# Performance work log

Measured on AMD Instinct MI355X. Metric: run time of the kernel, lower is better.

## Reference

```python
import jax, jax.numpy as jnp
import numpy as np

H, I, SI, E = 2048, 1408, 5632, 60
B, S = 1, 512


def setup_inputs() -> dict:
    key = jax.random.key(0)
    ks = jax.random.split(key, 9)
    sc = 0.02  # weight init scale for numerical stability
    return {
        "hidden_states": jax.random.normal(ks[0], (B, S, H), dtype=jnp.float32),
        "router_w": jax.random.normal(ks[1], (E, H), dtype=jnp.float32) * sc,
        "gate_w": jax.random.normal(ks[2], (E, I, H), dtype=jnp.float32) * sc,
        "up_w": jax.random.normal(ks[3], (E, I, H), dtype=jnp.float32) * sc,
        "down_w": jax.random.normal(ks[4], (E, H, I), dtype=jnp.float32) * sc,
        "sh_gate_w": jax.random.normal(ks[5], (SI, H), dtype=jnp.float32) * sc,
        "sh_up_w": jax.random.normal(ks[6], (SI, H), dtype=jnp.float32) * sc,
        "sh_down_w": jax.random.normal(ks[7], (H, SI), dtype=jnp.float32) * sc,
        "expert_gate_w": jax.random.normal(ks[8], (1, H), dtype=jnp.float32) * sc,
        "top_k": 4,
    }


NORM_TOPK_PROB = False  # Qwen1.5-MoE config


def reference(hidden_states, router_w, gate_w, up_w, down_w,
              sh_gate_w, sh_up_w, sh_down_w, expert_gate_w, top_k):
    b, s, h = hidden_states.shape
    x = hidden_states.reshape(-1, h)                      # [T, H]

    # --- router: softmax over all experts, then top-k sparse weights ---
    logits = x @ router_w.T                               # [T, E]
    probs = jax.nn.softmax(logits.astype(jnp.float32), axis=-1)
    vals, idx = jax.lax.top_k(probs, top_k)               # [T, k]
    if NORM_TOPK_PROB:
        vals = vals / jnp.sum(vals, axis=-1, keepdims=True)
    # scatter top-k weights back to dense [T, E] (zeros elsewhere)
    onehot = jax.nn.one_hot(idx, E, dtype=probs.dtype)    # [T, k, E]
    w = jnp.einsum('tke,tk->te', onehot, vals).astype(x.dtype)  # [T, E]

    # --- grouped GLU experts (dense-masked faithful reference) ---
    g = jnp.einsum('td,eid->tei', x, gate_w)              # [T, E, I]
    a = jax.nn.silu(g) * jnp.einsum('td,eid->tei', x, up_w)
    moe = jnp.einsum('tei,ehi,te->th', a, down_w, w)      # [T, H]

    # --- shared expert with sigmoid gate ---
    shared = (jax.nn.silu(x @ sh_gate_w.T) * (x @ sh_up_w.T)) @ sh_down_w.T
    shared = jax.nn.sigmoid(x @ expert_gate_w.T) * shared # [T,1]*[T,H]

    return (moe + shared).reshape(b, s, h)
```

## Files before the change

### kernel.cpp

```cpp
#include <hip/hip_runtime.h>
#include <hip/hip_bf16.h>
#include <stdint.h>

#define TOKENS 512
#define HDIM   2048
#define IDIM   1408
#define SIDIM  5632
#define NEXP   60
#define TOPK   4
#define NSLOTS (TOKENS*TOPK)
#define ROWPAD 64

#define VMWAIT(N) asm volatile("s_waitcnt vmcnt(" #N ")" ::: "memory")
#define SBAR()    asm volatile("s_barrier" ::: "memory")

typedef __attribute__((ext_vector_type(8))) short bf16x8;
typedef __attribute__((ext_vector_type(4))) float f32x4;

__device__ __forceinline__ short f2bf(float f){
  uint32_t u = __float_as_uint(f);
  u = (u + 0x7fffu + ((u >> 16) & 1u)) >> 16;
  return (short)(u & 0xffffu);
}

__device__ __forceinline__ bf16x8 pack8(float4 a, float4 b){
  bf16x8 r;
  r[0]=f2bf(a.x); r[1]=f2bf(a.y); r[2]=f2bf(a.z); r[3]=f2bf(a.w);
  r[4]=f2bf(b.x); r[5]=f2bf(b.y); r[6]=f2bf(b.z); r[7]=f2bf(b.w);
  return r;
}

__device__ __forceinline__ bf16x8 as_bf16x8(float4 v){
  union { float4 f; bf16x8 b; } u; u.f = v; return u.b;
}

__device__ __forceinline__ f32x4 zero4(){
  f32x4 z; z[0]=0.f; z[1]=0.f; z[2]=0.f; z[3]=0.f; return z;
}

__device__ __forceinline__ f32x4 mfma16(bf16x8 a, bf16x8 b, f32x4 c){
  return __builtin_amdgcn_mfma_f32_16x16x32_bf16(a, b, c, 0, 0, 0);
}

__device__ __forceinline__ void stage_w32(float4* tile, const float* __restrict__ W,
                                          int K, int k0, int tid){
  int l = tid & 63, wv = tid >> 6;
  #pragma unroll
  for (int j=0;j<2;j++){
    int u0 = j*256 + wv*64;
    int u  = u0 + l;
    int row = u >> 3;
    int lu  = ((u & 7) - (row & 7)) & 7;
    const float* src = W + (size_t)row*K + k0 + lu*4;
    __builtin_amdgcn_global_load_lds(
        (const __attribute__((address_space(1))) void*)src,
        (__attribute__((address_space(3))) void*)(tile + u0), 16, 0, 0);
  }
}

__device__ __forceinline__ bf16x8 read_wfrag32(const float4* tile, int r, int kq){
  int rot = r & 7;
  const float4* row = tile + (size_t)r*8;
  float4 f0 = row[(2*kq     + rot) & 7];
  float4 f1 = row[(2*kq + 1 + rot) & 7];
  return pack8(f0, f1);
}

__device__ __forceinline__ void stage_a32(float4* tile, const short* __restrict__ Arows,
                                          int K, int k0, int tid){
  int l = tid & 63, wv = tid >> 6;
  int u0 = wv*64;
  int u  = u0 + l;
  int row = u >> 2;
  int lu  = ((u & 3) - (row & 3)) & 3;
  const short* src = Arows + (size_t)row*K + k0 + lu*8;
  __builtin_amdgcn_global_load_lds(
      (const __attribute__((address_space(1))) void*)src,
      (__attribute__((address_space(3))) void*)(tile + u0), 16, 0, 0);
}

__device__ __forceinline__ void read_afrag32(const float4* tile, int c16, int kq,
                                             bf16x8* av){
  #pragma unroll
  for (int mf=0; mf<4; mf++){
    int row = c16 + 16*mf;
    av[mf] = as_bf16x8(tile[(size_t)row*4 + ((kq + row) & 3)]);
  }
}

__global__ __launch_bounds__(64) void router_kernel(
    const float* __restrict__ x, const float* __restrict__ rw,
    const float* __restrict__ egw, int* __restrict__ topk_idx,
    float* __restrict__ topk_w, float* __restrict__ gates,
    int* __restrict__ counts)
{
  int t = blockIdx.x;
  int lane = threadIdx.x;
  const float* xr = x + (size_t)t*HDIM;
  float xv[HDIM/64];
  #pragma unroll
  for (int i=0;i<HDIM/64;i++) xv[i] = xr[lane + 64*i];

  float mylogit = -1e30f;
  for (int e=0;e<NEXP;e++){
    const float* w = rw + (size_t)e*HDIM;
    float acc = 0.f;
    #pragma unroll
    for (int i=0;i<HDIM/64;i++) acc += xv[i]*w[lane+64*i];
    #pragma unroll
    for (int s=32;s>0;s>>=1) acc += __shfl_xor(acc, s);
    if (lane == e) mylogit = acc;
  }
  {
    float acc = 0.f;
    #pragma unroll
    for (int i=0;i<HDIM/64;i++) acc += xv[i]*egw[lane+64*i];
    #pragma unroll
    for (int s=32;s>0;s>>=1) acc += __shfl_xor(acc, s);
    if (lane == 0) gates[t] = 1.f/(1.f + __expf(-acc));
  }
  float m = mylogit;
  #pragma unroll
  for (int s=32;s>0;s>>=1) m = fmaxf(m, __shfl_xor(m, s));
  float p = (lane < NEXP) ? __expf(mylogit - m) : 0.f;
  float sum = p;
  #pragma unroll
  for (int s=32;s>0;s>>=1) sum += __shfl_xor(sum, s);
  float prob = p / sum;
  for (int k=0;k<TOPK;k++){
    float v = prob; int idx = lane;
    #pragma unroll
    for (int s=32;s>0;s>>=1){
      float ov = __shfl_xor(v, s); int oi = __shfl_xor(idx, s);
      if (ov > v || (ov == v && oi < idx)){ v = ov; idx = oi; }
    }
    if (lane == 0){
      topk_idx[t*TOPK+k] = idx;
      topk_w[t*TOPK+k]  = v;
      atomicAdd(&counts[idx], 1);
    }
    if (lane == idx) prob = -1e30f;
  }
}

__global__ void prefix_kernel(const int* __restrict__ counts, int* __restrict__ offsets)
{
  if (threadIdx.x == 0){
    int acc = 0;
    for (int e=0;e<NEXP;e++){ offsets[e] = acc; acc += counts[e]; }
    offsets[NEXP] = acc;
  }
}

__global__ __launch_bounds__(256) void scatter_kernel(
    const float* __restrict__ x, const int* __restrict__ topk_idx,
    const int* __restrict__ offsets, int* __restrict__ fill,
    int* __restrict__ slot_of, __hip_bfloat16* __restrict__ xg,
    __hip_bfloat16* __restrict__ xb)
{
  int t = blockIdx.x, tid = threadIdx.x;
  __shared__ int sl[TOPK];
  if (tid == 0){
    for (int k=0;k<TOPK;k++){
      int e = topk_idx[t*TOPK+k];
      int pos = atomicAdd(&fill[e], 1);
      int s = offsets[e] + pos;
      slot_of[t*TOPK+k] = s;
      sl[k] = s;
    }
  }
  __syncthreads();
  const float4* xr = (const float4*)(x + (size_t)t*HDIM);
  float4 v0 = xr[tid*2], v1 = xr[tid*2+1];
  bf16x8 b = pack8(v0, v1);
  *(bf16x8*)((short*)xb + (size_t)t*HDIM + tid*8) = b;
  #pragma unroll
  for (int k=0;k<TOPK;k++)
    *(bf16x8*)((short*)xg + (size_t)sl[k]*HDIM + tid*8) = b;
}

__global__ __launch_bounds__(256, 4) void gateup_all(
    const float* __restrict__ gW_e, const float* __restrict__ uW_e,
    const __hip_bfloat16* __restrict__ A_e, __hip_bfloat16* __restrict__ out_e,
    const float* __restrict__ gW_s, const float* __restrict__ uW_s,
    const __hip_bfloat16* __restrict__ A_s, __hip_bfloat16* __restrict__ out_s,
    const int* __restrict__ offsets)
{
  extern __shared__ __align__(16) char smem[];
  float4* G0 = (float4*)smem;
  float4* G1 = G0 + 512;
  float4* U0 = G1 + 512;
  float4* U1 = U0 + 512;
  float4* A0 = U1 + 512;
  float4* A1 = A0 + 256;

  int bid = blockIdx.x;
  int xcd = bid & 7, pos = bid >> 3;
  const float *Wg, *Wu; const short *Abase; short *outp;
  int NI, bx, m_start, m_end;
  if (pos < 88){
    bx = pos;
    Wg = gW_s; Wu = uW_s; Abase = (const short*)A_s; outp = (short*)out_s;
    NI = SIDIM;
    m_start = xcd*64; m_end = m_start + 64;
  } else {
    int q = xcd*165 + (pos - 88);
    int e = q/22; bx = q - e*22;
    size_t wo = (size_t)e * IDIM * HDIM;
    Wg = gW_e + wo; Wu = uW_e + wo;
    Abase = (const short*)A_e; outp = (short*)out_e;
    NI = IDIM;
    m_start = offsets[e]; m_end = offsets[e+1];
  }
  if (m_start >= m_end) return;
  const int K = HDIM;

  int tid  = threadIdx.x;
  int lane = tid & 63;
  int wv   = tid >> 6;
  int c16 = lane & 15, kq = lane >> 4;
  int wrow = bx*64 + wv*16 + c16;
  int r    = wv*16 + c16;
  const float* WgT = Wg + (size_t)(bx*64)*K;
  const float* WuT = Wu + (size_t)(bx*64)*K;

  for (int m0 = m_start; m0 < m_end; m0 += 64){
    int mrem = m_end - m0;
    const short* Ar = Abase + (size_t)m0*K;
    f32x4 accg[4], accu[4];
    #pragma unroll
    for (int i=0;i<4;i++){ accg[i] = zero4(); accu[i] = zero4(); }

    stage_w32(G0, WgT, K, 0, tid);
    stage_w32(U0, WuT, K, 0, tid);
    stage_a32(A0, Ar,  K, 0, tid);

    for (int k0 = 0; k0 < K; k0 += 64){
      stage_w32(G1, WgT, K, k0+32, tid);
      stage_w32(U1, WuT, K, k0+32, tid);
      stage_a32(A1, Ar,  K, k0+32, tid);
      VMWAIT(5); SBAR();
      {
        bf16x8 av[4];
        read_afrag32(A0, c16, kq, av);
        bf16x8 bg = read_wfrag32(G0, r, kq);
        bf16x8 bu = read_wfrag32(U0, r, kq);
        #pragma unroll
        for (int mf=0; mf<4; mf++){
          accg[mf] = mfma16(av[mf], bg, accg[mf]);
          accu[mf] = mfma16(av[mf], bu, accu[mf]);
        }
      }
      SBAR();
      if (k0 + 64 < K){
        stage_w32(G0, WgT, K, k0+64, tid);
        stage_w32(U0, WuT, K, k0+64, tid);
        stage_a32(A0, Ar,  K, k0+64, tid);
        VMWAIT(5);
      } else {
        VMWAIT(0);
      }
      SBAR();
      {
        bf16x8 av[4];
        read_afrag32(A1, c16, kq, av);
        bf16x8 bg = read_wfrag32(G1, r, kq);
        bf16x8 bu = read_wfrag32(U1, r, kq);
        #pragma unroll
        for (int mf=0; mf<4; mf++){
          accg[mf] = mfma16(av[mf], bg, accg[mf]);
          accu[mf] = mfma16(av[mf], bu, accu[mf]);
        }
      }
      SBAR();
    }

    #pragma unroll
    for (int mf=0; mf<4; mf++){
      #pragma unroll
      for (int j=0;j<4;j++){
        int mrow = mf*16 + kq*4 + j;
        if (mrow < mrem){
          float g = accg[mf][j], u = accu[mf][j];
          float s = g * u / (1.f + __expf(-g));
          outp[(size_t)(m0+mrow)*NI + wrow] = f2bf(s);
        }
      }
    }
  }
}

__global__ __launch_bounds__(256, 4) void down_all(
    const float* __restrict__ W_e, const __hip_bfloat16* __restrict__ A_e,
    float* __restrict__ out_e,
    const float* __restrict__ W_s, const __hip_bfloat16* __restrict__ A_s,
    float* __restrict__ out_s,
    const int* __restrict__ offsets)
{
  extern __shared__ __align__(16) char smem[];
  float4* W0 = (float4*)smem;
  float4* W1 = W0 + 512;
  float4* A0 = W1 + 512;
  float4* A1 = A0 + 256;

  int bid = blockIdx.x;
  int xcd = bid & 7, pos = bid >> 3;
  const float* W; const short* Abase; float* outp;
  int K, bx, m_start, m_end;
  if (pos < 32){
    bx = pos;
    W = W_s; Abase = (const short*)A_s; outp = out_s; K = SIDIM;
    m_start = xcd*64; m_end = m_start + 64;
  } else {
    int q = xcd*240 + (pos - 32);
    int e = q >> 5; bx = q & 31;
    W = W_e + (size_t)e * HDIM * IDIM;
    Abase = (const short*)A_e; outp = out_e; K = IDIM;
    m_start = offsets[e]; m_end = offsets[e+1];
  }
  if (m_start >= m_end) return;

  int tid  = threadIdx.x;
  int lane = tid & 63;
  int wv   = tid >> 6;
  int c16 = lane & 15, kq = lane >> 4;
  int wrow = bx*64 + wv*16 + c16;
  int r    = wv*16 + c16;
  const float* WT = W + (size_t)(bx*64)*K;

  for (int m0 = m_start; m0 < m_end; m0 += 64){
    int mrem = m_end - m0;
    const short* Ar = Abase + (size_t)m0*K;
    f32x4 acc[4];
    #pragma unroll
    for (int i=0;i<4;i++) acc[i] = zero4();

    stage_w32(W0, WT, K, 0, tid);
    stage_a32(A0, Ar, K, 0, tid);

    for (int k0 = 0; k0 < K; k0 += 64){
      stage_w32(W1, WT, K, k0+32, tid);
      stage_a32(A1, Ar, K, k0+32, tid);
      VMWAIT(3); SBAR();
      {
        bf16x8 av[4];
        read_afrag32(A0, c16, kq, av);
        bf16x8 b = read_wfrag32(W0, r, kq);
        #pragma unroll
        for (int mf=0; mf<4; mf++)
          acc[mf] = mfma16(av[mf], b, acc[mf]);
      }
      SBAR();
      if (k0 + 64 < K){
        stage_w32(W0, WT, K, k0+64, tid);
        stage_a32(A0, Ar, K, k0+64, tid);
        VMWAIT(3);
      } else {
        VMWAIT(0);
      }
      SBAR();
      {
        bf16x8 av[4];
        read_afrag32(A1, c16, kq, av);
        bf16x8 b = read_wfrag32(W1, r, kq);
        #pragma unroll
        for (int mf=0; mf<4; mf++)
          acc[mf] = mfma16(av[mf], b, acc[mf]);
      }
      SBAR();
    }

    #pragma unroll
    for (int mf=0; mf<4; mf++){
      #pragma unroll
      for (int j=0;j<4;j++){
        int mrow = mf*16 + kq*4 + j;
        if (mrow < mrem)
          outp[(size_t)(m0+mrow)*HDIM + wrow] = acc[mf][j];
      }
    }
  }
}

__global__ __launch_bounds__(256) void combine_kernel(
    const float* __restrict__ dslot, const float* __restrict__ shdown,
    const int* __restrict__ slot_of, const float* __restrict__ topw,
    const float* __restrict__ gates, float* __restrict__ out)
{
  int t = blockIdx.x, tid = threadIdx.x;
  int4  sl = ((const int4*)slot_of)[t];
  float4 w = ((const float4*)topw)[t];
  float sg = gates[t];
  const float* r0 = dslot + (size_t)sl.x*HDIM;
  const float* r1 = dslot + (size_t)sl.y*HDIM;
  const float* r2 = dslot + (size_t)sl.z*HDIM;
  const float* r3 = dslot + (size_t)sl.w*HDIM;
  const float* rs = shdown + (size_t)t*HDIM;
  float* o = out + (size_t)t*HDIM;
  #pragma unroll
  for (int it=0; it<HDIM/(256*4); ++it){
    int h = (tid + it*256) * 4;
    float4 a0 = *(const float4*)(r0+h);
    float4 a1 = *(const float4*)(r1+h);
    float4 a2 = *(const float4*)(r2+h);
    float4 a3 = *(const float4*)(r3+h);
    float4 as = *(const float4*)(rs+h);
    float4 r;
    r.x = w.x*a0.x + w.y*a1.x + w.z*a2.x + w.w*a3.x + sg*as.x;
    r.y = w.x*a0.y + w.y*a1.y + w.z*a2.y + w.w*a3.y + sg*as.y;
    r.z = w.x*a0.z + w.y*a1.z + w.z*a2.z + w.w*a3.z + sg*as.z;
    r.w = w.x*a0.w + w.y*a1.w + w.z*a2.w + w.w*a3.w + sg*as.w;
    *(float4*)(o+h) = r;
  }
}

extern "C" void kernel_launch(void* const* d_in, const int* in_sizes, int n_in,
                              void* d_out, int out_size, void* d_ws, size_t ws_size,
                              hipStream_t stream)
{
  const float* x         = (const float*)d_in[0];
  const float* router_w  = (const float*)d_in[1];
  const float* gate_w    = (const float*)d_in[2];
  const float* up_w      = (const float*)d_in[3];
  const float* down_w    = (const float*)d_in[4];
  const float* sh_gate_w = (const float*)d_in[5];
  const float* sh_up_w   = (const float*)d_in[6];
  const float* sh_down_w = (const float*)d_in[7];
  const float* eg_w      = (const float*)d_in[8];

  char* p = (char*)d_ws;
  auto alloc = [&](size_t bytes)->char*{
    char* r = p; p += (bytes + 255) & ~(size_t)255; return r;
  };
  int*   counts   = (int*)  alloc(NEXP*4);
  int*   fill     = (int*)  alloc(NEXP*4);
  int*   offsets  = (int*)  alloc((NEXP+1)*4);
  int*   topk_idx = (int*)  alloc(NSLOTS*4);
  float* topk_w   = (float*)alloc(NSLOTS*4);
  int*   slot_of  = (int*)  alloc(NSLOTS*4);
  float* gates    = (float*)alloc(TOKENS*4);
  __hip_bfloat16* xb    = (__hip_bfloat16*)alloc((size_t)TOKENS*HDIM*2);
  __hip_bfloat16* xg    = (__hip_bfloat16*)alloc((size_t)(NSLOTS+ROWPAD)*HDIM*2);
  __hip_bfloat16* act   = (__hip_bfloat16*)alloc((size_t)(NSLOTS+ROWPAD)*IDIM*2);
  __hip_bfloat16* shact = (__hip_bfloat16*)alloc((size_t)TOKENS*SIDIM*2);
  float* dslot  = (float*)alloc((size_t)NSLOTS*HDIM*4);
  float* shdown = (float*)alloc((size_t)TOKENS*HDIM*4);
  if ((size_t)(p - (char*)d_ws) > ws_size) return;

  hipMemsetAsync(counts, 0, NEXP*4, stream);
  hipMemsetAsync(fill,   0, NEXP*4, stream);

  router_kernel <<<TOKENS, 64, 0, stream>>>(x, router_w, eg_w, topk_idx, topk_w, gates, counts);
  prefix_kernel <<<1, 64, 0, stream>>>(counts, offsets);
  scatter_kernel<<<TOKENS, 256, 0, stream>>>(x, topk_idx, offsets, fill, slot_of, xg, xb);

  gateup_all<<<2024, 256, 40*1024, stream>>>(
      gate_w, up_w, xg, act,
      sh_gate_w, sh_up_w, xb, shact, offsets);

  down_all<<<2176, 256, 24*1024, stream>>>(
      down_w, act, dslot,
      sh_down_w, shact, shdown, offsets);

  combine_kernel<<<TOKENS, 256, 0, stream>>>(dslot, shdown, slot_of, topk_w, gates, (float*)d_out);
}
```

Before: 654.1 us.

## Fuse MoE pipeline into persistent cooperative megakernel with atomic work queues

Replaces the six-kernel launch sequence with a single cooperative persistent kernel. Stages are separated by grid.sync, and the gate/up and down GEMM tiles are claimed dynamically from eight per-XCD atomic work queues with work stealing. The prefix sum is folded into the scatter stage, and the two memsets are merged into one. This is meant to remove launch gaps and tail imbalance. In exchange it adds grid-barrier cost, caps concurrency at 1024 resident blocks, and raises register pressure in the merged kernel.

Measured after the change: 672.8 us. 1.03x slower.

```diff
diff --git a/kernel.cpp b/kernel.cpp
--- a/kernel.cpp
+++ b/kernel.cpp
@@ -1,6 +1,9 @@
 #include <hip/hip_runtime.h>
 #include <hip/hip_bf16.h>
+#include <hip/hip_cooperative_groups.h>
 #include <stdint.h>
+
+namespace cg = cooperative_groups;
 
 #define TOKENS 512
 #define HDIM   2048
@@ -10,6 +13,9 @@
 #define TOPK   4
 #define NSLOTS (TOKENS*TOPK)
 #define ROWPAD 64
+
+#define NQ_G 253
+#define NQ_D 272
 
 #define VMWAIT(N) asm volatile("s_waitcnt vmcnt(" #N ")" ::: "memory")
 #define SBAR()    asm volatile("s_barrier" ::: "memory")
@@ -88,22 +94,22 @@
   }
 }
 
-__global__ __launch_bounds__(64) void router_kernel(
-    const float* __restrict__ x, const float* __restrict__ rw,
-    const float* __restrict__ egw, int* __restrict__ topk_idx,
-    float* __restrict__ topk_w, float* __restrict__ gates,
-    int* __restrict__ counts)
-{
-  int t = blockIdx.x;
-  int lane = threadIdx.x;
-  const float* xr = x + (size_t)t*HDIM;
+struct MegaArgs {
+  const float *x, *rw, *gw, *uw, *dw, *sgw, *suw, *sdw, *egw;
+  int *counts, *fill, *offsets, *topk_idx, *slot_of, *qg, *qd, *mb;
+  float *topk_w, *gates, *dslot, *shdown, *out;
+  short *xb, *xg, *act, *shact;
+};
+
+__device__ __forceinline__ void router_body(const MegaArgs& a, int t, int lane){
+  const float* xr = a.x + (size_t)t*HDIM;
   float xv[HDIM/64];
   #pragma unroll
   for (int i=0;i<HDIM/64;i++) xv[i] = xr[lane + 64*i];
 
   float mylogit = -1e30f;
   for (int e=0;e<NEXP;e++){
-    const float* w = rw + (size_t)e*HDIM;
+    const float* w = a.rw + (size_t)e*HDIM;
     float acc = 0.f;
     #pragma unroll
     for (int i=0;i<HDIM/64;i++) acc += xv[i]*w[lane+64*i];
@@ -114,10 +120,10 @@
   {
     float acc = 0.f;
     #pragma unroll
-    for (int i=0;i<HDIM/64;i++) acc += xv[i]*egw[lane+64*i];
+    for (int i=0;i<HDIM/64;i++) acc += xv[i]*a.egw[lane+64*i];
     #pragma unroll
     for (int s=32;s>0;s>>=1) acc += __shfl_xor(acc, s);
-    if (lane == 0) gates[t] = 1.f/(1.f + __expf(-acc));
+    if (lane == 0) a.gates[t] = 1.f/(1.f + __expf(-acc));
   }
   float m = mylogit;
   #pragma unroll
@@ -135,58 +141,48 @@
       if (ov > v || (ov == v && oi < idx)){ v = ov; idx = oi; }
     }
     if (lane == 0){
-      topk_idx[t*TOPK+k] = idx;
-      topk_w[t*TOPK+k]  = v;
-      atomicAdd(&counts[idx], 1);
+      a.topk_idx[t*TOPK+k] = idx;
+      a.topk_w[t*TOPK+k]  = v;
+      atomicAdd(&a.counts[idx], 1);
     }
     if (lane == idx) prob = -1e30f;
   }
 }
 
-__global__ void prefix_kernel(const int* __restrict__ counts, int* __restrict__ offsets)
-{
-  if (threadIdx.x == 0){
-    int acc = 0;
-    for (int e=0;e<NEXP;e++){ offsets[e] = acc; acc += counts[e]; }
-    offsets[NEXP] = acc;
-  }
-}
-
-__global__ __launch_bounds__(256) void scatter_kernel(
-    const float* __restrict__ x, const int* __restrict__ topk_idx,
-    const int* __restrict__ offsets, int* __restrict__ fill,
-    int* __restrict__ slot_of, __hip_bfloat16* __restrict__ xg,
-    __hip_bfloat16* __restrict__ xb)
-{
-  int t = blockIdx.x, tid = threadIdx.x;
-  __shared__ int sl[TOPK];
+__device__ __forceinline__ void scatter_body(const MegaArgs& a, int t, int tid, int bid){
   if (tid == 0){
-    for (int k=0;k<TOPK;k++){
-      int e = topk_idx[t*TOPK+k];
-      int pos = atomicAdd(&fill[e], 1);
-      int s = offsets[e] + pos;
-      slot_of[t*TOPK+k] = s;
-      sl[k] = s;
-    }
+    int e0 = a.topk_idx[t*TOPK+0], e1 = a.topk_idx[t*TOPK+1];
+    int e2 = a.topk_idx[t*TOPK+2], e3 = a.topk_idx[t*TOPK+3];
+    int o0=0,o1=0,o2=0,o3=0, acc=0;
+    for (int e=0;e<NEXP;e++){
+      int c = a.counts[e];
+      if (bid == 0) a.offsets[e] = acc;
+      if (e==e0) o0=acc; if (e==e1) o1=acc;
+      if (e==e2) o2=acc; if (e==e3) o3=acc;
+      acc += c;
+    }
+    if (bid == 0) a.offsets[NEXP] = acc;
+    int s0 = o0 + atomicAdd(&a.fill[e0],1);
+    int s1 = o1 + atomicAdd(&a.fill[e1],1);
+    int s2 = o2 + atomicAdd(&a.fill[e2],1);
+    int s3 = o3 + atomicAdd(&a.fill[e3],1);
+    a.slot_of[t*TOPK+0]=s0; a.slot_of[t*TOPK+1]=s1;
+    a.slot_of[t*TOPK+2]=s2; a.slot_of[t*TOPK+3]=s3;
   }
   __syncthreads();
-  const float4* xr = (const float4*)(x + (size_t)t*HDIM);
+  int4 sl = ((const int4*)a.slot_of)[t];
+  const float4* xr = (const float4*)(a.x + (size_t)t*HDIM);
   float4 v0 = xr[tid*2], v1 = xr[tid*2+1];
   bf16x8 b = pack8(v0, v1);
-  *(bf16x8*)((short*)xb + (size_t)t*HDIM + tid*8) = b;
-  #pragma unroll
-  for (int k=0;k<TOPK;k++)
-    *(bf16x8*)((short*)xg + (size_t)sl[k]*HDIM + tid*8) = b;
-}
-
-__global__ __launch_bounds__(256, 4) void gateup_all(
-    const float* __restrict__ gW_e, const float* __restrict__ uW_e,
-    const __hip_bfloat16* __restrict__ A_e, __hip_bfloat16* __restrict__ out_e,
-    const float* __restrict__ gW_s, const float* __restrict__ uW_s,
-    const __hip_bfloat16* __restrict__ A_s, __hip_bfloat16* __restrict__ out_s,
-    const int* __restrict__ offsets)
-{
-  extern __shared__ __align__(16) char smem[];
+  *(bf16x8*)(a.xb + (size_t)t*HDIM + tid*8) = b;
+  *(bf16x8*)(a.xg + (size_t)sl.x*HDIM + tid*8) = b;
+  *(bf16x8*)(a.xg + (size_t)sl.y*HDIM + tid*8) = b;
+  *(bf16x8*)(a.xg + (size_t)sl.z*HDIM + tid*8) = b;
+  *(bf16x8*)(a.xg + (size_t)sl.w*HDIM + tid*8) = b;
+}
+
+__device__ __forceinline__ void gateup_item(const MegaArgs& a, char* smem,
+                                            int q, int pos, int tid){
   float4* G0 = (float4*)smem;
   float4* G1 = G0 + 512;
   float4* U0 = G1 + 512;
@@ -194,28 +190,23 @@
   float4* A0 = U1 + 512;
   float4* A1 = A0 + 256;
 
-  int bid = blockIdx.x;
-  int xcd = bid & 7, pos = bid >> 3;
-  const float *Wg, *Wu; const short *Abase; short *outp;
+  const float *Wg, *Wu; const short* Abase; short* outp;
   int NI, bx, m_start, m_end;
   if (pos < 88){
     bx = pos;
-    Wg = gW_s; Wu = uW_s; Abase = (const short*)A_s; outp = (short*)out_s;
-    NI = SIDIM;
-    m_start = xcd*64; m_end = m_start + 64;
+    Wg = a.sgw; Wu = a.suw; Abase = a.xb; outp = a.shact;
+    NI = SIDIM; m_start = q*64; m_end = m_start + 64;
   } else {
-    int q = xcd*165 + (pos - 88);
-    int e = q/22; bx = q - e*22;
+    int qq = q*165 + (pos - 88);
+    int e = qq/22; bx = qq - e*22;
     size_t wo = (size_t)e * IDIM * HDIM;
-    Wg = gW_e + wo; Wu = uW_e + wo;
-    Abase = (const short*)A_e; outp = (short*)out_e;
-    NI = IDIM;
-    m_start = offsets[e]; m_end = offsets[e+1];
+    Wg = a.gw + wo; Wu = a.uw + wo;
+    Abase = a.xg; outp = a.act;
+    NI = IDIM; m_start = a.offsets[e]; m_end = a.offsets[e+1];
   }
   if (m_start >= m_end) return;
   const int K = HDIM;
 
-  int tid  = threadIdx.x;
   int lane = tid & 63;
   int wv   = tid >> 6;
   int c16 = lane & 15, kq = lane >> 4;
@@ -290,37 +281,28 @@
   }
 }
 
-__global__ __launch_bounds__(256, 4) void down_all(
-    const float* __restrict__ W_e, const __hip_bfloat16* __restrict__ A_e,
-    float* __restrict__ out_e,
-    const float* __restrict__ W_s, const __hip_bfloat16* __restrict__ A_s,
-    float* __restrict__ out_s,
-    const int* __restrict__ offsets)
-{
-  extern __shared__ __align__(16) char smem[];
+__device__ __forceinline__ void down_item(const MegaArgs& a, char* smem,
+                                          int q, int pos, int tid){
   float4* W0 = (float4*)smem;
   float4* W1 = W0 + 512;
   float4* A0 = W1 + 512;
   float4* A1 = A0 + 256;
 
-  int bid = blockIdx.x;
-  int xcd = bid & 7, pos = bid >> 3;
   const float* W; const short* Abase; float* outp;
   int K, bx, m_start, m_end;
   if (pos < 32){
     bx = pos;
-    W = W_s; Abase = (const short*)A_s; outp = out_s; K = SIDIM;
-    m_start = xcd*64; m_end = m_start + 64;
+    W = a.sdw; Abase = a.shact; outp = a.shdown; K = SIDIM;
+    m_start = q*64; m_end = m_start + 64;
   } else {
-    int q = xcd*240 + (pos - 32);
-    int e = q >> 5; bx = q & 31;
-    W = W_e + (size_t)e * HDIM * IDIM;
-    Abase = (const short*)A_e; outp = out_e; K = IDIM;
-    m_start = offsets[e]; m_end = offsets[e+1];
+    int qq = q*240 + (pos - 32);
+    int e = qq >> 5; bx = qq & 31;
+    W = a.dw + (size_t)e * HDIM * IDIM;
+    Abase = a.act; outp = a.dslot; K = IDIM;
+    m_start = a.offsets[e]; m_end = a.offsets[e+1];
   }
   if (m_start >= m_end) return;
 
-  int tid  = threadIdx.x;
   int lane = tid & 63;
   int wv   = tid >> 6;
   int c16 = lane & 15, kq = lane >> 4;
@@ -382,21 +364,16 @@
   }
 }
 
-__global__ __launch_bounds__(256) void combine_kernel(
-    const float* __restrict__ dslot, const float* __restrict__ shdown,
-    const int* __restrict__ slot_of, const float* __restrict__ topw,
-    const float* __restrict__ gates, float* __restrict__ out)
-{
-  int t = blockIdx.x, tid = threadIdx.x;
-  int4  sl = ((const int4*)slot_of)[t];
-  float4 w = ((const float4*)topw)[t];
-  float sg = gates[t];
-  const float* r0 = dslot + (size_t)sl.x*HDIM;
-  const float* r1 = dslot + (size_t)sl.y*HDIM;
-  const float* r2 = dslot + (size_t)sl.z*HDIM;
-  const float* r3 = dslot + (size_t)sl.w*HDIM;
-  const float* rs = shdown + (size_t)t*HDIM;
-  float* o = out + (size_t)t*HDIM;
+__device__ __forceinline__ void combine_body(const MegaArgs& a, int t, int tid){
+  int4  sl = ((const int4*)a.slot_of)[t];
+  float4 w = ((const float4*)a.topk_w)[t];
+  float sg = a.gates[t];
+  const float* r0 = a.dslot + (size_t)sl.x*HDIM;
+  const float* r1 = a.dslot + (size_t)sl.y*HDIM;
+  const float* r2 = a.dslot + (size_t)sl.z*HDIM;
+  const float* r3 = a.dslot + (size_t)sl.w*HDIM;
+  const float* rs = a.shdown + (size_t)t*HDIM;
+  float* o = a.out + (size_t)t*HDIM;
   #pragma unroll
   for (int it=0; it<HDIM/(256*4); ++it){
     int h = (tid + it*256) * 4;
@@ -414,53 +391,182 @@
   }
 }
 
+__global__ __launch_bounds__(256, 4) void mega(MegaArgs a)
+{
+  extern __shared__ __align__(16) char smem[];
+  cg::grid_group grid = cg::this_grid();
+  int bid = blockIdx.x, tid = threadIdx.x;
+  int wv = tid >> 6, lane = tid & 63;
+
+  if (bid < 128) router_body(a, bid*4 + wv, lane);
+  __threadfence(); grid.sync();
+
+  if (bid < TOKENS) scatter_body(a, bid, tid, bid);
+  __threadfence(); grid.sync();
+
+  {
+    int myq = bid & 7;
+    for (int dq=0; dq<8; ++dq){
+      int q = (myq + dq) & 7;
+      while (true){
+        if (tid == 0) a.mb[bid] = atomicAdd(&a.qg[q], 1);
+        __syncthreads();
+        int pos = a.mb[bid];
+        if (pos >= NQ_G) break;
+        gateup_item(a, smem, q, pos, tid);
+        __syncthreads();
+      }
+    }
+  }
+  __threadfence(); grid.sync();
+
+  {
+    int myq = bid & 7;
+    for (int dq=0; dq<8; ++dq){
+      int q = (myq + dq) & 7;
+      while (true){
+        if (tid == 0) a.mb[bid] = atomicAdd(&a.qd[q], 1);
+        __syncthreads();
+        int pos = a.mb[bid];
+        if (pos >= NQ_D) break;
+        down_item(a, smem, q, pos, tid);
+        __syncthreads();
+      }
+    }
+  }
+  __threadfence(); grid.sync();
+
+  if (bid < TOKENS) combine_body(a, bid, tid);
+}
+
+__global__ __launch_bounds__(64) void router_kernel(
+    const float* __restrict__ x, const float* __restrict__ rw,
+    const float* __restrict__ egw, int* __restrict__ topk_idx,
+    float* __restrict__ topk_w, float* __restrict__ gates,
+    int* __restrict__ counts)
+{
+  MegaArgs a{}; a.x=x; a.rw=rw; a.egw=egw; a.topk_idx=topk_idx;
+  a.topk_w=topk_w; a.gates=gates; a.counts=counts;
+  router_body(a, blockIdx.x, threadIdx.x);
+}
+
+__global__ void prefix_kernel(const int* __restrict__ counts, int* __restrict__ offsets)
+{
+  if (threadIdx.x == 0){
+    int acc = 0;
+    for (int e=0;e<NEXP;e++){ offsets[e] = acc; acc += counts[e]; }
+    offsets[NEXP] = acc;
+  }
+}
+
+__global__ __launch_bounds__(256) void scatter_kernel(
+    const float* __restrict__ x, const int* __restrict__ topk_idx,
+    const int* __restrict__ offsets, int* __restrict__ fill,
+    int* __restrict__ slot_of, __hip_bfloat16* __restrict__ xg,
+    __hip_bfloat16* __restrict__ xb)
+{
+  int t = blockIdx.x, tid = threadIdx.x;
+  __shared__ int sl[TOPK];
+  if (tid == 0){
+    for (int k=0;k<TOPK;k++){
+      int e = topk_idx[t*TOPK+k];
+      int pos = atomicAdd(&fill[e], 1);
+      int s = offsets[e] + pos;
+      slot_of[t*TOPK+k] = s;
+      sl[k] = s;
+    }
+  }
+  __syncthreads();
+  const float4* xr = (const float4*)(x + (size_t)t*HDIM);
+  float4 v0 = xr[tid*2], v1 = xr[tid*2+1];
+  bf16x8 b = pack8(v0, v1);
+  *(bf16x8*)((short*)xb + (size_t)t*HDIM + tid*8) = b;
+  #pragma unroll
+  for (int k=0;k<TOPK;k++)
+    *(bf16x8*)((short*)xg + (size_t)sl[k]*HDIM + tid*8) = b;
+}
+
+__global__ __launch_bounds__(256, 4) void gateup_all(MegaArgs a)
+{
+  extern __shared__ __align__(16) char smem[];
+  int bid = blockIdx.x;
+  gateup_item(a, smem, bid & 7, bid >> 3, threadIdx.x);
+}
+
+__global__ __launch_bounds__(256, 4) void down_all(MegaArgs a)
+{
+  extern __shared__ __align__(16) char smem[];
+  int bid = blockIdx.x;
+  down_item(a, smem, bid & 7, bid >> 3, threadIdx.x);
+}
+
+__global__ __launch_bounds__(256) void combine_kernel(MegaArgs a)
+{
+  combine_body(a, blockIdx.x, threadIdx.x);
+}
+
 extern "C" void kernel_launch(void* const* d_in, const int* in_sizes, int n_in,
                               void* d_out, int out_size, void* d_ws, size_t ws_size,
                               hipStream_t stream)
 {
-  const float* x         = (const float*)d_in[0];
-  const float* router_w  = (const float*)d_in[1];
-  const float* gate_w    = (const float*)d_in[2];
-  const float* up_w      = (const float*)d_in[3];
-  const float* down_w    = (const float*)d_in[4];
-  const float* sh_gate_w = (const float*)d_in[5];
-  const float* sh_up_w   = (const float*)d_in[6];
-  const float* sh_down_w = (const float*)d_in[7];
-  const float* eg_w      = (const float*)d_in[8];
+  MegaArgs a;
+  a.x   = (const float*)d_in[0];
+  a.rw  = (const float*)d_in[1];
+  a.gw  = (const float*)d_in[2];
+  a.uw  = (const float*)d_in[3];
+  a.dw  = (const float*)d_in[4];
+  a.sgw = (const float*)d_in[5];
+  a.suw = (const float*)d_in[6];
+  a.sdw = (const float*)d_in[7];
+  a.egw = (const float*)d_in[8];
+  a.out = (float*)d_out;
 
   char* p = (char*)d_ws;
   auto alloc = [&](size_t bytes)->char*{
     char* r = p; p += (bytes + 255) & ~(size_t)255; return r;
   };
-  int*   counts   = (int*)  alloc(NEXP*4);
-  int*   fill     = (int*)  alloc(NEXP*4);
-  int*   offsets  = (int*)  alloc((NEXP+1)*4);
-  int*   topk_idx = (int*)  alloc(NSLOTS*4);
-  float* topk_w   = (float*)alloc(NSLOTS*4);
-  int*   slot_of  = (int*)  alloc(NSLOTS*4);
-  float* gates    = (float*)alloc(TOKENS*4);
-  __hip_bfloat16* xb    = (__hip_bfloat16*)alloc((size_t)TOKENS*HDIM*2);
-  __hip_bfloat16* xg    = (__hip_bfloat16*)alloc((size_t)(NSLOTS+ROWPAD)*HDIM*2);
-  __hip_bfloat16* act   = (__hip_bfloat16*)alloc((size_t)(NSLOTS+ROWPAD)*IDIM*2);
-  __hip_bfloat16* shact = (__hip_bfloat16*)alloc((size_t)TOKENS*SIDIM*2);
-  float* dslot  = (float*)alloc((size_t)NSLOTS*HDIM*4);
-  float* shdown = (float*)alloc((size_t)TOKENS*HDIM*4);
+  int* zblock   = (int*)alloc((NEXP+NEXP+8+8)*4);
+  a.counts = zblock;
+  a.fill   = zblock + NEXP;
+  a.qg     = zblock + 2*NEXP;
+  a.qd     = zblock + 2*NEXP + 8;
+  a.offsets  = (int*)  alloc((NEXP+1)*4);
+  a.topk_idx = (int*)  alloc(NSLOTS*4);
+  a.topk_w   = (float*)alloc(NSLOTS*4);
+  a.slot_of  = (int*)  alloc(NSLOTS*4);
+  a.gates    = (float*)alloc(TOKENS*4);
+  a.mb       = (int*)  alloc(1024*4);
+  a.xb    = (short*)alloc((size_t)TOKENS*HDIM*2);
+  a.xg    = (short*)alloc((size_t)(NSLOTS+ROWPAD)*HDIM*2);
+  a.act   = (short*)alloc((size_t)(NSLOTS+ROWPAD)*IDIM*2);
+  a.shact = (short*)alloc((size_t)TOKENS*SIDIM*2);
+  a.dslot  = (float*)alloc((size_t)NSLOTS*HDIM*4);
+  a.shdown = (float*)alloc((size_t)TOKENS*HDIM*4);
   if ((size_t)(p - (char*)d_ws) > ws_size) return;
 
-  hipMemsetAsync(counts, 0, NEXP*4, stream);
-  hipMemsetAsync(fill,   0, NEXP*4, stream);
-
-  router_kernel <<<TOKENS, 64, 0, stream>>>(x, router_w, eg_w, topk_idx, topk_w, gates, counts);
-  prefix_kernel <<<1, 64, 0, stream>>>(counts, offsets);
-  scatter_kernel<<<TOKENS, 256, 0, stream>>>(x, topk_idx, offsets, fill, slot_of, xg, xb);
-
-  gateup_all<<<2024, 256, 40*1024, stream>>>(
-      gate_w, up_w, xg, act,
-      sh_gate_w, sh_up_w, xb, shact, offsets);
-
-  down_all<<<2176, 256, 24*1024, stream>>>(
-      down_w, act, dslot,
-      sh_down_w, shact, shdown, offsets);
-
-  combine_kernel<<<TOKENS, 256, 0, stream>>>(dslot, shdown, slot_of, topk_w, gates, (float*)d_out);
-}
+  hipMemsetAsync(zblock, 0, (NEXP+NEXP+8+8)*4, stream);
+
+  int nb = 0;
+  hipError_t qerr = hipOccupancyMaxActiveBlocksPerMultiprocessor(&nb, mega, 256, 40*1024);
+  int gridsz = 0;
+  if (qerr == hipSuccess){
+    if (nb >= 4) gridsz = 1024;
+    else if (nb == 3) gridsz = 768;
+  }
+  if (gridsz){
+    void* kargs[] = { (void*)&a };
+    hipError_t err = hipLaunchCooperativeKernel((const void*)mega, dim3(gridsz),
+                                                dim3(256), kargs, 40*1024, stream);
+    if (err == hipSuccess) return;
+  }
+
+  router_kernel <<<TOKENS, 64, 0, stream>>>(a.x, a.rw, a.egw, a.topk_idx,
+                                            a.topk_w, a.gates, a.counts);
+  prefix_kernel <<<1, 64, 0, stream>>>(a.counts, a.offsets);
+  scatter_kernel<<<TOKENS, 256, 0, stream>>>(a.x, a.topk_idx, a.offsets, a.fill,
+                                             a.slot_of, (__hip_bfloat16*)a.xg,
+                                             (__hip_bfloat16*)a.xb);
+  gateup_all<<<8*NQ_G, 256, 40*1024, stream>>>(a);
+  down_all  <<<8*NQ_D, 256, 24*1024, stream>>>(a);
+  combine_kernel<<<TOKENS, 256, 0, stream>>>(a);
+}
```
